# Performance work log

Measured on AMD Instinct MI355X. Metric: run time of the kernel, lower is better.

## Reference

```python
import jax, jax.numpy as jnp
import numpy as np

DIM_Q = 512
DIM_K = 512
D_Q4 = float(DIM_Q) ** 0.25  # torch: dim_q ** (1/4)
D_K4 = float(DIM_K) ** 0.25


def setup_inputs() -> dict:
    key = jax.random.key(0)
    ks = jax.random.split(key, 9)
    B, N, D_IN = 8, 4096, 512
    s_in = 1.0 / np.sqrt(D_IN)
    return {
        "x_q": jax.random.normal(ks[0], (B, N, D_IN), jnp.float32),
        "x_k": jax.random.normal(ks[1], (B, N, D_IN), jnp.float32),
        "x_v": jax.random.normal(ks[2], (B, N, D_IN), jnp.float32),
        # Linear params stored as [in, out] for x @ W + b
        "W_q": jax.random.uniform(ks[3], (D_IN, DIM_Q), jnp.float32, -s_in, s_in),
        "b_q": jax.random.uniform(ks[4], (DIM_Q,), jnp.float32, -s_in, s_in),
        "W_k": jax.random.uniform(ks[5], (D_IN, DIM_K), jnp.float32, -s_in, s_in),
        "b_k": jax.random.uniform(ks[6], (DIM_K,), jnp.float32, -s_in, s_in),
        "W_v": jax.random.uniform(ks[7], (D_IN, DIM_K), jnp.float32, -s_in, s_in),
        "b_v": jax.random.uniform(ks[8], (DIM_K,), jnp.float32, -s_in, s_in),
    }


def reference(x_q, x_k, x_v, W_q, b_q, W_k, b_k, W_v, b_v):
    Q = x_q @ W_q + b_q          # [B, n, dq]
    K = x_k @ W_k + b_k          # [B, n, dk]
    V = x_v @ W_v + b_v          # [B, n, dk]
    # softmax_row: over sequence axis (dim=-2) of Q
    A = jax.nn.softmax(Q / D_Q4, axis=-2)          # [B, n, dq]
    # softmax_col on K^T (dim=-1) == softmax over sequence axis of K
    Ks = jax.nn.softmax(K / D_K4, axis=-2)         # [B, n, dk]
    Bm = jnp.einsum("bnd,bne->bde", Ks, V)        # [B, dk, dk]
    Z = jnp.einsum("bnd,bde->bne", A, Bm)         # [B, n, dk]
    return Z
```

## Files before the change

### kernel.cpp

```cpp
#include <hip/hip_runtime.h>
#include <hip/hip_bf16.h>


typedef __bf16 bf16_t;
typedef __attribute__((ext_vector_type(8))) __bf16 bf16x8;
typedef __attribute__((ext_vector_type(4))) float f32x4;

#define MFMA_BF16 __builtin_amdgcn_mfma_f32_16x16x32_bf16

__device__ inline void async_ld16(const void* g, void* l) {
  __builtin_amdgcn_global_load_lds(
      (const __attribute__((address_space(1))) void*)g,
      (__attribute__((address_space(3))) void*)l, 16, 0, 0);
}

#define INV_D4 0.2102241038134287f

__global__ __launch_bounds__(256) void wt_kernel(
    const float* __restrict__ Wq, const float* __restrict__ Wk,
    const float* __restrict__ Wv, bf16_t* __restrict__ Wt) {
  const int z = blockIdx.z;
  const float* W = (z == 0) ? Wq : (z == 1) ? Wk : Wv;
  bf16_t* O = Wt + (size_t)z * 262144;
  __shared__ __align__(16) bf16_t tile[64 * 72];
  const int t = threadIdx.x;
  const int r = t >> 2;
  const int c4 = (t & 3) * 16;
  const int in0 = blockIdx.x * 64, out0 = blockIdx.y * 64;
  const float* src = W + (size_t)(in0 + r) * 512 + out0 + c4;
#pragma unroll
  for (int i = 0; i < 4; ++i) {
    float4 f = ((const float4*)src)[i];
    tile[(c4 + i * 4 + 0) * 72 + r] = (__bf16)f.x;
    tile[(c4 + i * 4 + 1) * 72 + r] = (__bf16)f.y;
    tile[(c4 + i * 4 + 2) * 72 + r] = (__bf16)f.z;
    tile[(c4 + i * 4 + 3) * 72 + r] = (__bf16)f.w;
  }
  __syncthreads();
  bf16x8* dst = (bf16x8*)(O + (size_t)(out0 + r) * 512 + in0 + c4);
  const bf16x8* s = (const bf16x8*)(tile + r * 72 + c4);
  dst[0] = s[0];
  dst[1] = s[1];
}

__global__ __launch_bounds__(256, 2) void proj_q(
    const float* __restrict__ Xq, const bf16_t* __restrict__ Wt,
    const float* __restrict__ bias, bf16_t* __restrict__ Eq,
    float* __restrict__ Sq) {
  __shared__ __align__(16) bf16_t Xs[4096];
  __shared__ __align__(16) bf16_t Ws[8192];

  const int t = threadIdx.x;
  const int lane = t & 63, w = t >> 6;
  const int quad = lane >> 4, l15 = lane & 15;
  const int m0 = blockIdx.x * 128;
  const int n0 = blockIdx.y * 256;
  const int m_off = (w & 1) * 64, n_off = (w >> 1) * 128;

  f32x4 acc[4][8];
  const f32x4 zero4 = {0.f, 0.f, 0.f, 0.f};
#pragma unroll
  for (int i = 0; i < 4; ++i)
#pragma unroll
    for (int j = 0; j < 8; ++j) acc[i][j] = zero4;

  const int ar = t >> 1;
  const int ac = (t & 1) * 16;
  const float* abase = Xq + (size_t)(m0 + ar) * 512 + ac;

  float4 f0 = ((const float4*)abase)[0];
  float4 f1 = ((const float4*)abase)[1];
  float4 f2 = ((const float4*)abase)[2];
  float4 f3 = ((const float4*)abase)[3];

  for (int ks = 0; ks < 16; ++ks) {
    bf16x8 p0, p1;
    p0[0] = (__bf16)f0.x; p0[1] = (__bf16)f0.y; p0[2] = (__bf16)f0.z; p0[3] = (__bf16)f0.w;
    p0[4] = (__bf16)f1.x; p0[5] = (__bf16)f1.y; p0[6] = (__bf16)f1.z; p0[7] = (__bf16)f1.w;
    p1[0] = (__bf16)f2.x; p1[1] = (__bf16)f2.y; p1[2] = (__bf16)f2.z; p1[3] = (__bf16)f2.w;
    p1[4] = (__bf16)f3.x; p1[5] = (__bf16)f3.y; p1[6] = (__bf16)f3.z; p1[7] = (__bf16)f3.w;
    ((bf16x8*)Xs)[(ac >> 3) * 128 + ar] = p0;
    ((bf16x8*)Xs)[((ac >> 3) + 1) * 128 + ar] = p1;

#pragma unroll
    for (int i = 0; i < 4; ++i) {
      const int j = w * 4 + i;
      const int k8 = j >> 2;
      const int r = ((j & 3) << 6) + lane;
      async_ld16(Wt + (size_t)(n0 + r) * 512 + ks * 32 + k8 * 8, Ws + j * 512);
    }
    __syncthreads();

    bf16x8 af[4], bfr[8];
#pragma unroll
    for (int mi = 0; mi < 4; ++mi)
      af[mi] = ((const bf16x8*)Xs)[quad * 128 + m_off + mi * 16 + l15];
#pragma unroll
    for (int ni = 0; ni < 8; ++ni)
      bfr[ni] = ((const bf16x8*)Ws)[quad * 256 + n_off + ni * 16 + l15];

    if (ks < 15) {
      const float4* p = (const float4*)(abase + (ks + 1) * 32);
      f0 = p[0]; f1 = p[1]; f2 = p[2]; f3 = p[3];
    }

#pragma unroll
    for (int mi = 0; mi < 4; ++mi)
#pragma unroll
      for (int ni = 0; ni < 8; ++ni)
        acc[mi][ni] = MFMA_BF16(af[mi], bfr[ni], acc[mi][ni], 0, 0, 0);
    __syncthreads();
  }

  const int b = m0 >> 12;
  float cs[8];
#pragma unroll
  for (int ni = 0; ni < 8; ++ni) cs[ni] = 0.f;
#pragma unroll
  for (int ni = 0; ni < 8; ++ni) {
    const int col = n0 + n_off + ni * 16 + l15;
    const float bv_ = bias[col];
#pragma unroll
    for (int mi = 0; mi < 4; ++mi)
#pragma unroll
      for (int r = 0; r < 4; ++r) {
        const int row = m0 + m_off + mi * 16 + quad * 4 + r;
        float v = __expf((acc[mi][ni][r] + bv_) * INV_D4);
        Eq[(size_t)row * 512 + col] = (bf16_t)v;
        cs[ni] += v;
      }
  }
#pragma unroll
  for (int ni = 0; ni < 8; ++ni) {
    cs[ni] += __shfl_xor(cs[ni], 16);
    cs[ni] += __shfl_xor(cs[ni], 32);
  }
  if (lane < 16) {
#pragma unroll
    for (int ni = 0; ni < 8; ++ni)
      atomicAdd(&Sq[b * 512 + n0 + n_off + ni * 16 + lane], cs[ni]);
  }
}

__global__ __launch_bounds__(256, 2) void proj_kv(
    const float* __restrict__ xk, const float* __restrict__ xv,
    const bf16_t* __restrict__ Wt, const float* __restrict__ bk,
    const float* __restrict__ bv, bf16_t* __restrict__ Ft,
    bf16_t* __restrict__ Vt) {
  const int z = blockIdx.z + 1;
  const float* X = (z == 1) ? xk : xv;
  const float* bias = (z == 1) ? bk : bv;
  const bf16_t* W = Wt + (size_t)z * 262144;
  bf16_t* Out = (z == 1) ? Ft : Vt;
  const bool expm = (z == 1);

  __shared__ __align__(16) bf16_t Xs[4096];
  __shared__ __align__(16) bf16_t Ws[8192];

  const int t = threadIdx.x;
  const int lane = t & 63, w = t >> 6;
  const int quad = lane >> 4, l15 = lane & 15;
  const int ng = blockIdx.x * 128;
  const int w0 = blockIdx.y * 256;
  const int m_off = (w & 1) * 128, n_off = (w >> 1) * 64;

  f32x4 acc[8][4];
  const f32x4 zero4 = {0.f, 0.f, 0.f, 0.f};
#pragma unroll
  for (int i = 0; i < 8; ++i)
#pragma unroll
    for (int j = 0; j < 4; ++j) acc[i][j] = zero4;

  const int br = t >> 1;
  const int bc = (t & 1) * 16;
  const float* bbase = X + (size_t)(ng + br) * 512 + bc;

  float4 f0 = ((const float4*)bbase)[0];
  float4 f1 = ((const float4*)bbase)[1];
  float4 f2 = ((const float4*)bbase)[2];
  float4 f3 = ((const float4*)bbase)[3];

  for (int ks = 0; ks < 16; ++ks) {
    bf16x8 p0, p1;
    p0[0] = (__bf16)f0.x; p0[1] = (__bf16)f0.y; p0[2] = (__bf16)f0.z; p0[3] = (__bf16)f0.w;
    p0[4] = (__bf16)f1.x; p0[5] = (__bf16)f1.y; p0[6] = (__bf16)f1.z; p0[7] = (__bf16)f1.w;
    p1[0] = (__bf16)f2.x; p1[1] = (__bf16)f2.y; p1[2] = (__bf16)f2.z; p1[3] = (__bf16)f2.w;
    p1[4] = (__bf16)f3.x; p1[5] = (__bf16)f3.y; p1[6] = (__bf16)f3.z; p1[7] = (__bf16)f3.w;
    ((bf16x8*)Xs)[(bc >> 3) * 128 + br] = p0;
    ((bf16x8*)Xs)[((bc >> 3) + 1) * 128 + br] = p1;

#pragma unroll
    for (int i = 0; i < 4; ++i) {
      const int j = w * 4 + i;
      const int k8 = j >> 2;
      const int r = ((j & 3) << 6) + lane;
      async_ld16(W + (size_t)(w0 + r) * 512 + ks * 32 + k8 * 8, Ws + j * 512);
    }
    __syncthreads();

    bf16x8 af[8], bfr[4];
#pragma unroll
    for (int mi = 0; mi < 8; ++mi)
      af[mi] = ((const bf16x8*)Ws)[quad * 256 + m_off + mi * 16 + l15];
#pragma unroll
    for (int ni = 0; ni < 4; ++ni)
      bfr[ni] = ((const bf16x8*)Xs)[quad * 128 + n_off + ni * 16 + l15];

    if (ks < 15) {
      const float4* p = (const float4*)(bbase + (ks + 1) * 32);
      f0 = p[0]; f1 = p[1]; f2 = p[2]; f3 = p[3];
    }

#pragma unroll
    for (int mi = 0; mi < 8; ++mi)
#pragma unroll
      for (int ni = 0; ni < 4; ++ni)
        acc[mi][ni] = MFMA_BF16(af[mi], bfr[ni], acc[mi][ni], 0, 0, 0);
    __syncthreads();
  }

  const int b = ng >> 12;
  const int nl0 = (ng & 4095) + n_off;
#pragma unroll
  for (int mi = 0; mi < 8; ++mi)
#pragma unroll
    for (int r = 0; r < 4; ++r) {
      const int d = w0 + m_off + mi * 16 + quad * 4 + r;
      const float bv_ = bias[d];
      bf16_t* rowp = Out + (size_t)b * 2097152 + (size_t)d * 4096 + nl0;
#pragma unroll
      for (int ni = 0; ni < 4; ++ni) {
        float v = acc[mi][ni][r] + bv_;
        if (expm) v = __expf(v * INV_D4);
        rowp[ni * 16 + l15] = (bf16_t)v;
      }
    }
}

__global__ __launch_bounds__(256) void sk_kernel(const bf16_t* __restrict__ Ft,
                                                 float* __restrict__ Sk) {
  const int row = blockIdx.x * 4 + (threadIdx.x >> 6);
  const int lane = threadIdx.x & 63;
  const bf16x8* p = (const bf16x8*)(Ft + (size_t)row * 4096) + lane;
  float s = 0.f;
#pragma unroll
  for (int j = 0; j < 8; ++j) {
    bf16x8 v = p[j * 64];
#pragma unroll
    for (int e = 0; e < 8; ++e) s += (float)v[e];
  }
#pragma unroll
  for (int m = 1; m <= 32; m <<= 1) s += __shfl_xor(s, m);
  if (lane == 0) Sk[row] = s;
}

__global__ __launch_bounds__(256, 2) void bm_gemm(
    const bf16_t* __restrict__ Ft, const bf16_t* __restrict__ Vt,
    float* __restrict__ Bmp) {
  const int b = blockIdx.z >> 1;
  const int s = blockIdx.z & 1;
  const int d0 = blockIdx.x * 128;
  const int e0 = blockIdx.y * 128;
  const bf16_t* A = Ft + (size_t)b * 2097152;
  const bf16_t* B = Vt + (size_t)b * 2097152;
  float* out = Bmp + ((size_t)s * 8 + b) * 262144;

  __shared__ __align__(16) bf16_t As[4096];
  __shared__ __align__(16) bf16_t Bs[4096];

  const int t = threadIdx.x;
  const int lane = t & 63, w = t >> 6;
  const int quad = lane >> 4, l15 = lane & 15;
  const int m_off = (w & 1) * 64, n_off = (w >> 1) * 64;

  f32x4 acc[4][4];
  const f32x4 zero4 = {0.f, 0.f, 0.f, 0.f};
#pragma unroll
  for (int i = 0; i < 4; ++i)
#pragma unroll
    for (int j = 0; j < 4; ++j) acc[i][j] = zero4;

  for (int ks = 0; ks < 64; ++ks) {
    const int k0 = s * 2048 + ks * 32;
#pragma unroll
    for (int i = 0; i < 2; ++i) {
      const int j = w * 2 + i;
      const int k8 = j >> 1;
      const int r = ((j & 1) << 6) + lane;
      async_ld16(A + (size_t)(d0 + r) * 4096 + k0 + k8 * 8, As + j * 512);
      async_ld16(B + (size_t)(e0 + r) * 4096 + k0 + k8 * 8, Bs + j * 512);
    }
    __syncthreads();
    bf16x8 af[4], bfr[4];
#pragma unroll
    for (int mi = 0; mi < 4; ++mi)
      af[mi] = ((const bf16x8*)As)[quad * 128 + m_off + mi * 16 + l15];
#pragma unroll
    for (int ni = 0; ni < 4; ++ni)
      bfr[ni] = ((const bf16x8*)Bs)[quad * 128 + n_off + ni * 16 + l15];
#pragma unroll
    for (int mi = 0; mi < 4; ++mi)
#pragma unroll
      for (int ni = 0; ni < 4; ++ni)
        acc[mi][ni] = MFMA_BF16(af[mi], bfr[ni], acc[mi][ni], 0, 0, 0);
    __syncthreads();
  }

#pragma unroll
  for (int mi = 0; mi < 4; ++mi)
#pragma unroll
    for (int ni = 0; ni < 4; ++ni) {
      const int ecol = e0 + n_off + ni * 16 + l15;
#pragma unroll
      for (int r = 0; r < 4; ++r) {
        const int drow = d0 + m_off + mi * 16 + quad * 4 + r;
        out[(size_t)drow * 512 + ecol] = acc[mi][ni][r];
      }
    }
}

__global__ __launch_bounds__(256) void scale_kernel(
    const float* __restrict__ Bmp, const float* __restrict__ Sq,
    const float* __restrict__ Sk, bf16_t* __restrict__ Ct) {
  const int b = blockIdx.z;
  const int d0 = blockIdx.x * 64, e0 = blockIdx.y * 64;
  __shared__ __align__(16) bf16_t tile[64 * 72];
  const int t = threadIdx.x;
  const int r = t >> 2;
  const int c4 = (t & 3) * 16;
  const int d = d0 + r;
  const float f = 1.0f / (Sq[b * 512 + d] * Sk[b * 512 + d]);
  const float* p0 = Bmp + (size_t)b * 262144 + (size_t)d * 512 + e0 + c4;
  const float* p1 = p0 + 2097152;
#pragma unroll
  for (int i = 0; i < 4; ++i) {
    float4 v0 = ((const float4*)p0)[i];
    float4 v1 = ((const float4*)p1)[i];
    tile[(c4 + i * 4 + 0) * 72 + r] = (__bf16)((v0.x + v1.x) * f);
    tile[(c4 + i * 4 + 1) * 72 + r] = (__bf16)((v0.y + v1.y) * f);
    tile[(c4 + i * 4 + 2) * 72 + r] = (__bf16)((v0.z + v1.z) * f);
    tile[(c4 + i * 4 + 3) * 72 + r] = (__bf16)((v0.w + v1.w) * f);
  }
  __syncthreads();
  bf16x8* dst = (bf16x8*)(Ct + (size_t)b * 262144 + (size_t)(e0 + r) * 512 + d0 + c4);
  const bf16x8* s = (const bf16x8*)(tile + r * 72 + c4);
  dst[0] = s[0];
  dst[1] = s[1];
}

__global__ __launch_bounds__(256, 2) void z_gemm(
    const bf16_t* __restrict__ Eq, const bf16_t* __restrict__ Ct,
    float* __restrict__ out) {
  __shared__ __align__(16) bf16_t As[4096];
  __shared__ __align__(16) bf16_t Bs[8192];

  const int t = threadIdx.x;
  const int lane = t & 63, w = t >> 6;
  const int quad = lane >> 4, l15 = lane & 15;
  const int m0 = blockIdx.x * 128;
  const int n0 = blockIdx.y * 256;
  const int batch = m0 >> 12;
  const bf16_t* Bt = Ct + (size_t)batch * 262144;
  const int m_off = (w & 1) * 64, n_off = (w >> 1) * 128;

  f32x4 acc[4][8];
  const f32x4 zero4 = {0.f, 0.f, 0.f, 0.f};
#pragma unroll
  for (int i = 0; i < 4; ++i)
#pragma unroll
    for (int j = 0; j < 8; ++j) acc[i][j] = zero4;

  for (int ks = 0; ks < 16; ++ks) {
    const int k0 = ks * 32;
#pragma unroll
    for (int i = 0; i < 2; ++i) {
      const int j = w * 2 + i;
      const int k8 = j >> 1;
      const int r = ((j & 1) << 6) + lane;
      async_ld16(Eq + (size_t)(m0 + r) * 512 + k0 + k8 * 8, As + j * 512);
    }
#pragma unroll
    for (int i = 0; i < 4; ++i) {
      const int j = w * 4 + i;
      const int k8 = j >> 2;
      const int r = ((j & 3) << 6) + lane;
      async_ld16(Bt + (size_t)(n0 + r) * 512 + k0 + k8 * 8, Bs + j * 512);
    }
    __syncthreads();
    bf16x8 af[4], bfr[8];
#pragma unroll
    for (int mi = 0; mi < 4; ++mi)
      af[mi] = ((const bf16x8*)As)[quad * 128 + m_off + mi * 16 + l15];
#pragma unroll
    for (int ni = 0; ni < 8; ++ni)
      bfr[ni] = ((const bf16x8*)Bs)[quad * 256 + n_off + ni * 16 + l15];
#pragma unroll
    for (int mi = 0; mi < 4; ++mi)
#pragma unroll
      for (int ni = 0; ni < 8; ++ni)
        acc[mi][ni] = MFMA_BF16(af[mi], bfr[ni], acc[mi][ni], 0, 0, 0);
    __syncthreads();
  }

#pragma unroll
  for (int mi = 0; mi < 4; ++mi)
#pragma unroll
    for (int ni = 0; ni < 8; ++ni) {
      const int col = n0 + n_off + ni * 16 + l15;
#pragma unroll
      for (int r = 0; r < 4; ++r) {
        const int row = m0 + m_off + mi * 16 + quad * 4 + r;
        out[(size_t)row * 512 + col] = acc[mi][ni][r];
      }
    }
}

extern "C" void kernel_launch(void* const* d_in, const int* in_sizes, int n_in,
                              void* d_out, int out_size, void* d_ws,
                              size_t ws_size, hipStream_t stream) {
  const float* xq = (const float*)d_in[0];
  const float* xk = (const float*)d_in[1];
  const float* xv = (const float*)d_in[2];
  const float* Wq = (const float*)d_in[3];
  const float* bq = (const float*)d_in[4];
  const float* Wk = (const float*)d_in[5];
  const float* bk = (const float*)d_in[6];
  const float* Wv = (const float*)d_in[7];
  const float* bv = (const float*)d_in[8];
  float* out = (float*)d_out;

  char* ws = (char*)d_ws;
  bf16_t* Eq = (bf16_t*)(ws + 0);
  bf16_t* Ft = (bf16_t*)(ws + 33554432);
  bf16_t* Vt = (bf16_t*)(ws + 67108864);
  float* Bmp = (float*)(ws + 100663296);
  bf16_t* Wt = (bf16_t*)(ws + 117440512);
  float* Sq = (float*)(ws + 119013376);
  float* Sk = (float*)(ws + 119029760);
  bf16_t* Ct = (bf16_t*)(ws + 33554432);

  hipMemsetAsync(Sq, 0, 16384, stream);

  wt_kernel<<<dim3(8, 8, 3), 256, 0, stream>>>(Wq, Wk, Wv, Wt);
  proj_q<<<dim3(256, 2), 256, 0, stream>>>(xq, Wt, bq, Eq, Sq);
  proj_kv<<<dim3(256, 2, 2), 256, 0, stream>>>(xk, xv, Wt, bk, bv, Ft, Vt);
  sk_kernel<<<dim3(1024), 256, 0, stream>>>(Ft, Sk);
  bm_gemm<<<dim3(4, 4, 16), 256, 0, stream>>>(Ft, Vt, Bmp);
  scale_kernel<<<dim3(8, 8, 8), 256, 0, stream>>>(Bmp, Sq, Sk, Ct);
  z_gemm<<<dim3(256, 2), 256, 0, stream>>>(Eq, Ct, out);
}
```

Measured before the change: 389.7 us.

## Double-buffer GEMM mainloops, load weights to registers, widen split-K in bm_gemm

The three projection-style GEMMs (proj_q, proj_kv, z_gemm) now read weight fragments straight from global memory into registers instead of staging them in LDS. They also double-buffer the activation tile in LDS with a two-step register prefetch, so only one barrier is needed per k-step. bm_gemm gets double-buffered async LDS loads and a split-K factor that rises to 4 when the workspace is large enough, with scale_kernel summing a variable number of partials. The aim is to hide global-load latency and raise occupancy/parallelism, at the cost of more registers and redundant weight loads across blocks.

```diff
diff --git a/kernel.cpp b/kernel.cpp
--- a/kernel.cpp
+++ b/kernel.cpp
@@ -15,6 +15,30 @@
 }
 
 #define INV_D4 0.2102241038134287f
+
+#define BAR_LGKM()                                        \
+  do {                                                    \
+    asm volatile("s_waitcnt lgkmcnt(0)" ::: "memory");    \
+    __builtin_amdgcn_s_barrier();                         \
+  } while (0)
+
+#define BAR_VM_LGKM()                                             \
+  do {                                                            \
+    asm volatile("s_waitcnt vmcnt(0) lgkmcnt(0)" ::: "memory");   \
+    __builtin_amdgcn_s_barrier();                                 \
+  } while (0)
+
+__device__ inline void cvt_store(bf16_t* dst, int c0, int ar, const float4& f0,
+                                 const float4& f1, const float4& f2,
+                                 const float4& f3) {
+  bf16x8 p0, p1;
+  p0[0] = (__bf16)f0.x; p0[1] = (__bf16)f0.y; p0[2] = (__bf16)f0.z; p0[3] = (__bf16)f0.w;
+  p0[4] = (__bf16)f1.x; p0[5] = (__bf16)f1.y; p0[6] = (__bf16)f1.z; p0[7] = (__bf16)f1.w;
+  p1[0] = (__bf16)f2.x; p1[1] = (__bf16)f2.y; p1[2] = (__bf16)f2.z; p1[3] = (__bf16)f2.w;
+  p1[4] = (__bf16)f3.x; p1[5] = (__bf16)f3.y; p1[6] = (__bf16)f3.z; p1[7] = (__bf16)f3.w;
+  ((bf16x8*)dst)[c0 * 128 + ar] = p0;
+  ((bf16x8*)dst)[(c0 + 1) * 128 + ar] = p1;
+}
 
 __global__ __launch_bounds__(256) void wt_kernel(
     const float* __restrict__ Wq, const float* __restrict__ Wk,
@@ -47,98 +71,97 @@
     const float* __restrict__ Xq, const bf16_t* __restrict__ Wt,
     const float* __restrict__ bias, bf16_t* __restrict__ Eq,
     float* __restrict__ Sq) {
-  __shared__ __align__(16) bf16_t Xs[4096];
-  __shared__ __align__(16) bf16_t Ws[8192];
+  __shared__ __align__(16) bf16_t Xs[2][4096];
 
   const int t = threadIdx.x;
   const int lane = t & 63, w = t >> 6;
   const int quad = lane >> 4, l15 = lane & 15;
   const int m0 = blockIdx.x * 128;
-  const int n0 = blockIdx.y * 256;
-  const int m_off = (w & 1) * 64, n_off = (w >> 1) * 128;
-
-  f32x4 acc[4][8];
+  const int n0 = blockIdx.y * 256 + w * 64;
+
+  f32x4 acc[8][4];
   const f32x4 zero4 = {0.f, 0.f, 0.f, 0.f};
 #pragma unroll
-  for (int i = 0; i < 4; ++i)
-#pragma unroll
-    for (int j = 0; j < 8; ++j) acc[i][j] = zero4;
+  for (int i = 0; i < 8; ++i)
+#pragma unroll
+    for (int j = 0; j < 4; ++j) acc[i][j] = zero4;
 
   const int ar = t >> 1;
-  const int ac = (t & 1) * 16;
-  const float* abase = Xq + (size_t)(m0 + ar) * 512 + ac;
-
-  float4 f0 = ((const float4*)abase)[0];
-  float4 f1 = ((const float4*)abase)[1];
-  float4 f2 = ((const float4*)abase)[2];
-  float4 f3 = ((const float4*)abase)[3];
-
+  const int c0 = (t & 1) * 2;
+  const float* abase = Xq + (size_t)(m0 + ar) * 512 + (t & 1) * 16;
+  const bf16_t* wbase = Wt + (size_t)(n0 + l15) * 512 + quad * 8;
+
+  float4 fb[2][4];
+  bf16x8 wr[2][4];
+
+  {
+    const float4* p = (const float4*)abase;
+    fb[1][0] = p[0]; fb[1][1] = p[1]; fb[1][2] = p[2]; fb[1][3] = p[3];
+  }
+#pragma unroll
+  for (int ni = 0; ni < 4; ++ni)
+    wr[0][ni] = *(const bf16x8*)(wbase + ni * 8192);
+  {
+    const float4* p = (const float4*)(abase + 32);
+    fb[0][0] = p[0]; fb[0][1] = p[1]; fb[0][2] = p[2]; fb[0][3] = p[3];
+  }
+  cvt_store(Xs[0], c0, ar, fb[1][0], fb[1][1], fb[1][2], fb[1][3]);
+  {
+    const float4* p = (const float4*)(abase + 64);
+    fb[1][0] = p[0]; fb[1][1] = p[1]; fb[1][2] = p[2]; fb[1][3] = p[3];
+  }
+  BAR_LGKM();
+
+#pragma unroll
   for (int ks = 0; ks < 16; ++ks) {
-    bf16x8 p0, p1;
-    p0[0] = (__bf16)f0.x; p0[1] = (__bf16)f0.y; p0[2] = (__bf16)f0.z; p0[3] = (__bf16)f0.w;
-    p0[4] = (__bf16)f1.x; p0[5] = (__bf16)f1.y; p0[6] = (__bf16)f1.z; p0[7] = (__bf16)f1.w;
-    p1[0] = (__bf16)f2.x; p1[1] = (__bf16)f2.y; p1[2] = (__bf16)f2.z; p1[3] = (__bf16)f2.w;
-    p1[4] = (__bf16)f3.x; p1[5] = (__bf16)f3.y; p1[6] = (__bf16)f3.z; p1[7] = (__bf16)f3.w;
-    ((bf16x8*)Xs)[(ac >> 3) * 128 + ar] = p0;
-    ((bf16x8*)Xs)[((ac >> 3) + 1) * 128 + ar] = p1;
-
-#pragma unroll
-    for (int i = 0; i < 4; ++i) {
-      const int j = w * 4 + i;
-      const int k8 = j >> 2;
-      const int r = ((j & 3) << 6) + lane;
-      async_ld16(Wt + (size_t)(n0 + r) * 512 + ks * 32 + k8 * 8, Ws + j * 512);
-    }
-    __syncthreads();
-
-    bf16x8 af[4], bfr[8];
-#pragma unroll
-    for (int mi = 0; mi < 4; ++mi)
-      af[mi] = ((const bf16x8*)Xs)[quad * 128 + m_off + mi * 16 + l15];
-#pragma unroll
-    for (int ni = 0; ni < 8; ++ni)
-      bfr[ni] = ((const bf16x8*)Ws)[quad * 256 + n_off + ni * 16 + l15];
-
+    const int p = ks & 1;
+    bf16x8 af[8];
+#pragma unroll
+    for (int mi = 0; mi < 8; ++mi)
+      af[mi] = ((const bf16x8*)Xs[p])[quad * 128 + mi * 16 + l15];
     if (ks < 15) {
-      const float4* p = (const float4*)(abase + (ks + 1) * 32);
-      f0 = p[0]; f1 = p[1]; f2 = p[2]; f3 = p[3];
-    }
-
-#pragma unroll
-    for (int mi = 0; mi < 4; ++mi)
-#pragma unroll
-      for (int ni = 0; ni < 8; ++ni)
-        acc[mi][ni] = MFMA_BF16(af[mi], bfr[ni], acc[mi][ni], 0, 0, 0);
-    __syncthreads();
+      cvt_store(Xs[p ^ 1], c0, ar, fb[p][0], fb[p][1], fb[p][2], fb[p][3]);
+#pragma unroll
+      for (int ni = 0; ni < 4; ++ni)
+        wr[p ^ 1][ni] = *(const bf16x8*)(wbase + ni * 8192 + (ks + 1) * 32);
+      if (ks < 13) {
+        const float4* pp = (const float4*)(abase + (ks + 3) * 32);
+        fb[p][0] = pp[0]; fb[p][1] = pp[1]; fb[p][2] = pp[2]; fb[p][3] = pp[3];
+      }
+    }
+#pragma unroll
+    for (int mi = 0; mi < 8; ++mi)
+#pragma unroll
+      for (int ni = 0; ni < 4; ++ni)
+        acc[mi][ni] = MFMA_BF16(af[mi], wr[p][ni], acc[mi][ni], 0, 0, 0);
+    if (ks < 15) BAR_LGKM();
   }
 
   const int b = m0 >> 12;
-  float cs[8];
-#pragma unroll
-  for (int ni = 0; ni < 8; ++ni) cs[ni] = 0.f;
-#pragma unroll
-  for (int ni = 0; ni < 8; ++ni) {
-    const int col = n0 + n_off + ni * 16 + l15;
+  float cs[4] = {0.f, 0.f, 0.f, 0.f};
+#pragma unroll
+  for (int ni = 0; ni < 4; ++ni) {
+    const int col = n0 + ni * 16 + l15;
     const float bv_ = bias[col];
 #pragma unroll
-    for (int mi = 0; mi < 4; ++mi)
+    for (int mi = 0; mi < 8; ++mi)
 #pragma unroll
       for (int r = 0; r < 4; ++r) {
-        const int row = m0 + m_off + mi * 16 + quad * 4 + r;
+        const int row = m0 + mi * 16 + quad * 4 + r;
         float v = __expf((acc[mi][ni][r] + bv_) * INV_D4);
         Eq[(size_t)row * 512 + col] = (bf16_t)v;
         cs[ni] += v;
       }
   }
 #pragma unroll
-  for (int ni = 0; ni < 8; ++ni) {
+  for (int ni = 0; ni < 4; ++ni) {
     cs[ni] += __shfl_xor(cs[ni], 16);
     cs[ni] += __shfl_xor(cs[ni], 32);
   }
   if (lane < 16) {
 #pragma unroll
-    for (int ni = 0; ni < 8; ++ni)
-      atomicAdd(&Sq[b * 512 + n0 + n_off + ni * 16 + lane], cs[ni]);
+    for (int ni = 0; ni < 4; ++ni)
+      atomicAdd(&Sq[b * 512 + n0 + ni * 16 + lane], cs[ni]);
   }
 }
 
@@ -154,82 +177,83 @@
   bf16_t* Out = (z == 1) ? Ft : Vt;
   const bool expm = (z == 1);
 
-  __shared__ __align__(16) bf16_t Xs[4096];
-  __shared__ __align__(16) bf16_t Ws[8192];
+  __shared__ __align__(16) bf16_t Xs[2][4096];
 
   const int t = threadIdx.x;
   const int lane = t & 63, w = t >> 6;
   const int quad = lane >> 4, l15 = lane & 15;
   const int ng = blockIdx.x * 128;
-  const int w0 = blockIdx.y * 256;
-  const int m_off = (w & 1) * 128, n_off = (w >> 1) * 64;
-
-  f32x4 acc[8][4];
+  const int d0 = blockIdx.y * 256 + w * 64;
+
+  f32x4 acc[4][8];
   const f32x4 zero4 = {0.f, 0.f, 0.f, 0.f};
 #pragma unroll
-  for (int i = 0; i < 8; ++i)
-#pragma unroll
-    for (int j = 0; j < 4; ++j) acc[i][j] = zero4;
-
-  const int br = t >> 1;
-  const int bc = (t & 1) * 16;
-  const float* bbase = X + (size_t)(ng + br) * 512 + bc;
-
-  float4 f0 = ((const float4*)bbase)[0];
-  float4 f1 = ((const float4*)bbase)[1];
-  float4 f2 = ((const float4*)bbase)[2];
-  float4 f3 = ((const float4*)bbase)[3];
-
+  for (int i = 0; i < 4; ++i)
+#pragma unroll
+    for (int j = 0; j < 8; ++j) acc[i][j] = zero4;
+
+  const int ar = t >> 1;
+  const int c0 = (t & 1) * 2;
+  const float* bbase = X + (size_t)(ng + ar) * 512 + (t & 1) * 16;
+  const bf16_t* wbase = W + (size_t)(d0 + l15) * 512 + quad * 8;
+
+  float4 fb[2][4];
+  bf16x8 wr[2][4];
+
+  {
+    const float4* p = (const float4*)bbase;
+    fb[1][0] = p[0]; fb[1][1] = p[1]; fb[1][2] = p[2]; fb[1][3] = p[3];
+  }
+#pragma unroll
+  for (int mi = 0; mi < 4; ++mi)
+    wr[0][mi] = *(const bf16x8*)(wbase + mi * 8192);
+  {
+    const float4* p = (const float4*)(bbase + 32);
+    fb[0][0] = p[0]; fb[0][1] = p[1]; fb[0][2] = p[2]; fb[0][3] = p[3];
+  }
+  cvt_store(Xs[0], c0, ar, fb[1][0], fb[1][1], fb[1][2], fb[1][3]);
+  {
+    const float4* p = (const float4*)(bbase + 64);
+    fb[1][0] = p[0]; fb[1][1] = p[1]; fb[1][2] = p[2]; fb[1][3] = p[3];
+  }
+  BAR_LGKM();
+
+#pragma unroll
   for (int ks = 0; ks < 16; ++ks) {
-    bf16x8 p0, p1;
-    p0[0] = (__bf16)f0.x; p0[1] = (__bf16)f0.y; p0[2] = (__bf16)f0.z; p0[3] = (__bf16)f0.w;
-    p0[4] = (__bf16)f1.x; p0[5] = (__bf16)f1.y; p0[6] = (__bf16)f1.z; p0[7] = (__bf16)f1.w;
-    p1[0] = (__bf16)f2.x; p1[1] = (__bf16)f2.y; p1[2] = (__bf16)f2.z; p1[3] = (__bf16)f2.w;
-    p1[4] = (__bf16)f3.x; p1[5] = (__bf16)f3.y; p1[6] = (__bf16)f3.z; p1[7] = (__bf16)f3.w;
-    ((bf16x8*)Xs)[(bc >> 3) * 128 + br] = p0;
-    ((bf16x8*)Xs)[((bc >> 3) + 1) * 128 + br] = p1;
-
-#pragma unroll
-    for (int i = 0; i < 4; ++i) {
-      const int j = w * 4 + i;
-      const int k8 = j >> 2;
-      const int r = ((j & 3) << 6) + lane;
-      async_ld16(W + (size_t)(w0 + r) * 512 + ks * 32 + k8 * 8, Ws + j * 512);
-    }
-    __syncthreads();
-
-    bf16x8 af[8], bfr[4];
-#pragma unroll
-    for (int mi = 0; mi < 8; ++mi)
-      af[mi] = ((const bf16x8*)Ws)[quad * 256 + m_off + mi * 16 + l15];
-#pragma unroll
-    for (int ni = 0; ni < 4; ++ni)
-      bfr[ni] = ((const bf16x8*)Xs)[quad * 128 + n_off + ni * 16 + l15];
-
+    const int p = ks & 1;
+    bf16x8 bx[8];
+#pragma unroll
+    for (int ni = 0; ni < 8; ++ni)
+      bx[ni] = ((const bf16x8*)Xs[p])[quad * 128 + ni * 16 + l15];
     if (ks < 15) {
-      const float4* p = (const float4*)(bbase + (ks + 1) * 32);
-      f0 = p[0]; f1 = p[1]; f2 = p[2]; f3 = p[3];
-    }
-
-#pragma unroll
-    for (int mi = 0; mi < 8; ++mi)
-#pragma unroll
-      for (int ni = 0; ni < 4; ++ni)
-        acc[mi][ni] = MFMA_BF16(af[mi], bfr[ni], acc[mi][ni], 0, 0, 0);
-    __syncthreads();
+      cvt_store(Xs[p ^ 1], c0, ar, fb[p][0], fb[p][1], fb[p][2], fb[p][3]);
+#pragma unroll
+      for (int mi = 0; mi < 4; ++mi)
+        wr[p ^ 1][mi] = *(const bf16x8*)(wbase + mi * 8192 + (ks + 1) * 32);
+      if (ks < 13) {
+        const float4* pp = (const float4*)(bbase + (ks + 3) * 32);
+        fb[p][0] = pp[0]; fb[p][1] = pp[1]; fb[p][2] = pp[2]; fb[p][3] = pp[3];
+      }
+    }
+#pragma unroll
+    for (int mi = 0; mi < 4; ++mi)
+#pragma unroll
+      for (int ni = 0; ni < 8; ++ni)
+        acc[mi][ni] = MFMA_BF16(wr[p][mi], bx[ni], acc[mi][ni], 0, 0, 0);
+    if (ks < 15) BAR_LGKM();
   }
 
   const int b = ng >> 12;
-  const int nl0 = (ng & 4095) + n_off;
-#pragma unroll
-  for (int mi = 0; mi < 8; ++mi)
+  const int nl0 = (ng & 4095);
+#pragma unroll
+  for (int mi = 0; mi < 4; ++mi)
 #pragma unroll
     for (int r = 0; r < 4; ++r) {
-      const int d = w0 + m_off + mi * 16 + quad * 4 + r;
+      const int d = d0 + mi * 16 + quad * 4 + r;
       const float bv_ = bias[d];
       bf16_t* rowp = Out + (size_t)b * 2097152 + (size_t)d * 4096 + nl0;
 #pragma unroll
-      for (int ni = 0; ni < 4; ++ni) {
+      for (int ni = 0; ni < 8; ++ni) {
         float v = acc[mi][ni][r] + bv_;
         if (expm) v = __expf(v * INV_D4);
         rowp[ni * 16 + l15] = (bf16_t)v;
@@ -256,23 +280,27 @@
 
 __global__ __launch_bounds__(256, 2) void bm_gemm(
     const bf16_t* __restrict__ Ft, const bf16_t* __restrict__ Vt,
-    float* __restrict__ Bmp) {
-  const int b = blockIdx.z >> 1;
-  const int s = blockIdx.z & 1;
+    float* __restrict__ Bmp, int S) {
+  const int b = blockIdx.z / S;
+  const int s = blockIdx.z - b * S;
   const int d0 = blockIdx.x * 128;
   const int e0 = blockIdx.y * 128;
   const bf16_t* A = Ft + (size_t)b * 2097152;
   const bf16_t* B = Vt + (size_t)b * 2097152;
   float* out = Bmp + ((size_t)s * 8 + b) * 262144;
 
-  __shared__ __align__(16) bf16_t As[4096];
-  __shared__ __align__(16) bf16_t Bs[4096];
+  __shared__ __align__(16) bf16_t As[2][4096];
+  __shared__ __align__(16) bf16_t Bs[2][4096];
 
   const int t = threadIdx.x;
   const int lane = t & 63, w = t >> 6;
   const int quad = lane >> 4, l15 = lane & 15;
   const int m_off = (w & 1) * 64, n_off = (w >> 1) * 64;
 
+  const int kper = 4096 / S;
+  const int KS = kper >> 5;
+  const int kbase = s * kper;
+
   f32x4 acc[4][4];
   const f32x4 zero4 = {0.f, 0.f, 0.f, 0.f};
 #pragma unroll
@@ -280,30 +308,38 @@
 #pragma unroll
     for (int j = 0; j < 4; ++j) acc[i][j] = zero4;
 
-  for (int ks = 0; ks < 64; ++ks) {
-    const int k0 = s * 2048 + ks * 32;
+  const int j0 = w * 2;
+  auto stage = [&](int buf, int ks) {
 #pragma unroll
     for (int i = 0; i < 2; ++i) {
-      const int j = w * 2 + i;
+      const int j = j0 + i;
       const int k8 = j >> 1;
       const int r = ((j & 1) << 6) + lane;
-      async_ld16(A + (size_t)(d0 + r) * 4096 + k0 + k8 * 8, As + j * 512);
-      async_ld16(B + (size_t)(e0 + r) * 4096 + k0 + k8 * 8, Bs + j * 512);
-    }
-    __syncthreads();
+      const int kel = kbase + ks * 32 + k8 * 8;
+      async_ld16(A + (size_t)(d0 + r) * 4096 + kel, &As[buf][j * 512]);
+      async_ld16(B + (size_t)(e0 + r) * 4096 + kel, &Bs[buf][j * 512]);
+    }
+  };
+
+  stage(0, 0);
+  BAR_VM_LGKM();
+
+  for (int ks = 0; ks < KS; ++ks) {
+    const int p = ks & 1;
+    if (ks + 1 < KS) stage(p ^ 1, ks + 1);
     bf16x8 af[4], bfr[4];
 #pragma unroll
     for (int mi = 0; mi < 4; ++mi)
-      af[mi] = ((const bf16x8*)As)[quad * 128 + m_off + mi * 16 + l15];
+      af[mi] = ((const bf16x8*)As[p])[quad * 128 + m_off + mi * 16 + l15];
 #pragma unroll
     for (int ni = 0; ni < 4; ++ni)
-      bfr[ni] = ((const bf16x8*)Bs)[quad * 128 + n_off + ni * 16 + l15];
+      bfr[ni] = ((const bf16x8*)Bs[p])[quad * 128 + n_off + ni * 16 + l15];
 #pragma unroll
     for (int mi = 0; mi < 4; ++mi)
 #pragma unroll
       for (int ni = 0; ni < 4; ++ni)
         acc[mi][ni] = MFMA_BF16(af[mi], bfr[ni], acc[mi][ni], 0, 0, 0);
-    __syncthreads();
+    if (ks + 1 < KS) BAR_VM_LGKM();
   }
 
 #pragma unroll
@@ -321,7 +357,7 @@
 
 __global__ __launch_bounds__(256) void scale_kernel(
     const float* __restrict__ Bmp, const float* __restrict__ Sq,
-    const float* __restrict__ Sk, bf16_t* __restrict__ Ct) {
+    const float* __restrict__ Sk, bf16_t* __restrict__ Ct, int S) {
   const int b = blockIdx.z;
   const int d0 = blockIdx.x * 64, e0 = blockIdx.y * 64;
   __shared__ __align__(16) bf16_t tile[64 * 72];
@@ -331,85 +367,100 @@
   const int d = d0 + r;
   const float f = 1.0f / (Sq[b * 512 + d] * Sk[b * 512 + d]);
   const float* p0 = Bmp + (size_t)b * 262144 + (size_t)d * 512 + e0 + c4;
-  const float* p1 = p0 + 2097152;
 #pragma unroll
   for (int i = 0; i < 4; ++i) {
-    float4 v0 = ((const float4*)p0)[i];
-    float4 v1 = ((const float4*)p1)[i];
-    tile[(c4 + i * 4 + 0) * 72 + r] = (__bf16)((v0.x + v1.x) * f);
-    tile[(c4 + i * 4 + 1) * 72 + r] = (__bf16)((v0.y + v1.y) * f);
-    tile[(c4 + i * 4 + 2) * 72 + r] = (__bf16)((v0.z + v1.z) * f);
-    tile[(c4 + i * 4 + 3) * 72 + r] = (__bf16)((v0.w + v1.w) * f);
+    float sx = 0.f, sy = 0.f, sz = 0.f, sw = 0.f;
+    for (int sp = 0; sp < S; ++sp) {
+      float4 v = ((const float4*)(p0 + (size_t)sp * 2097152))[i];
+      sx += v.x; sy += v.y; sz += v.z; sw += v.w;
+    }
+    tile[(c4 + i * 4 + 0) * 72 + r] = (__bf16)(sx * f);
+    tile[(c4 + i * 4 + 1) * 72 + r] = (__bf16)(sy * f);
+    tile[(c4 + i * 4 + 2) * 72 + r] = (__bf16)(sz * f);
+    tile[(c4 + i * 4 + 3) * 72 + r] = (__bf16)(sw * f);
   }
   __syncthreads();
   bf16x8* dst = (bf16x8*)(Ct + (size_t)b * 262144 + (size_t)(e0 + r) * 512 + d0 + c4);
-  const bf16x8* s = (const bf16x8*)(tile + r * 72 + c4);
-  dst[0] = s[0];
-  dst[1] = s[1];
+  const bf16x8* sptr = (const bf16x8*)(tile + r * 72 + c4);
+  dst[0] = sptr[0];
+  dst[1] = sptr[1];
 }
 
 __global__ __launch_bounds__(256, 2) void z_gemm(
     const bf16_t* __restrict__ Eq, const bf16_t* __restrict__ Ct,
     float* __restrict__ out) {
-  __shared__ __align__(16) bf16_t As[4096];
-  __shared__ __align__(16) bf16_t Bs[8192];
+  __shared__ __align__(16) bf16_t Xs[2][4096];
 
   const int t = threadIdx.x;
   const int lane = t & 63, w = t >> 6;
   const int quad = lane >> 4, l15 = lane & 15;
   const int m0 = blockIdx.x * 128;
-  const int n0 = blockIdx.y * 256;
+  const int n0 = blockIdx.y * 256 + w * 64;
   const int batch = m0 >> 12;
   const bf16_t* Bt = Ct + (size_t)batch * 262144;
-  const int m_off = (w & 1) * 64, n_off = (w >> 1) * 128;
-
-  f32x4 acc[4][8];
+
+  f32x4 acc[8][4];
   const f32x4 zero4 = {0.f, 0.f, 0.f, 0.f};
 #pragma unroll
-  for (int i = 0; i < 4; ++i)
-#pragma unroll
-    for (int j = 0; j < 8; ++j) acc[i][j] = zero4;
-
+  for (int i = 0; i < 8; ++i)
+#pragma unroll
+    for (int j = 0; j < 4; ++j) acc[i][j] = zero4;
+
+  const int ar = t >> 1;
+  const int c0 = (t & 1) * 2;
+  const bf16_t* abase = Eq + (size_t)(m0 + ar) * 512 + (t & 1) * 16;
+  const bf16_t* wbase = Bt + (size_t)(n0 + l15) * 512 + quad * 8;
+
+  bf16x8 eb[2][2];
+  bf16x8 wr[2][4];
+
+  eb[1][0] = *(const bf16x8*)abase;
+  eb[1][1] = *(const bf16x8*)(abase + 8);
+#pragma unroll
+  for (int ni = 0; ni < 4; ++ni)
+    wr[0][ni] = *(const bf16x8*)(wbase + ni * 8192);
+  eb[0][0] = *(const bf16x8*)(abase + 32);
+  eb[0][1] = *(const bf16x8*)(abase + 40);
+  ((bf16x8*)Xs[0])[c0 * 128 + ar] = eb[1][0];
+  ((bf16x8*)Xs[0])[(c0 + 1) * 128 + ar] = eb[1][1];
+  eb[1][0] = *(const bf16x8*)(abase + 64);
+  eb[1][1] = *(const bf16x8*)(abase + 72);
+  BAR_LGKM();
+
+#pragma unroll
   for (int ks = 0; ks < 16; ++ks) {
-    const int k0 = ks * 32;
-#pragma unroll
-    for (int i = 0; i < 2; ++i) {
-      const int j = w * 2 + i;
-      const int k8 = j >> 1;
-      const int r = ((j & 1) << 6) + lane;
-      async_ld16(Eq + (size_t)(m0 + r) * 512 + k0 + k8 * 8, As + j * 512);
-    }
-#pragma unroll
-    for (int i = 0; i < 4; ++i) {
-      const int j = w * 4 + i;
-      const int k8 = j >> 2;
-      const int r = ((j & 3) << 6) + lane;
-      async_ld16(Bt + (size_t)(n0 + r) * 512 + k0 + k8 * 8, Bs + j * 512);
-    }
-    __syncthreads();
-    bf16x8 af[4], bfr[8];
-#pragma unroll
-    for (int mi = 0; mi < 4; ++mi)
-      af[mi] = ((const bf16x8*)As)[quad * 128 + m_off + mi * 16 + l15];
-#pragma unroll
-    for (int ni = 0; ni < 8; ++ni)
-      bfr[ni] = ((const bf16x8*)Bs)[quad * 256 + n_off + ni * 16 + l15];
-#pragma unroll
-    for (int mi = 0; mi < 4; ++mi)
-#pragma unroll
-      for (int ni = 0; ni < 8; ++ni)
-        acc[mi][ni] = MFMA_BF16(af[mi], bfr[ni], acc[mi][ni], 0, 0, 0);
-    __syncthreads();
-  }
-
-#pragma unroll
-  for (int mi = 0; mi < 4; ++mi)
-#pragma unroll
-    for (int ni = 0; ni < 8; ++ni) {
-      const int col = n0 + n_off + ni * 16 + l15;
+    const int p = ks & 1;
+    bf16x8 af[8];
+#pragma unroll
+    for (int mi = 0; mi < 8; ++mi)
+      af[mi] = ((const bf16x8*)Xs[p])[quad * 128 + mi * 16 + l15];
+    if (ks < 15) {
+      ((bf16x8*)Xs[p ^ 1])[c0 * 128 + ar] = eb[p][0];
+      ((bf16x8*)Xs[p ^ 1])[(c0 + 1) * 128 + ar] = eb[p][1];
+#pragma unroll
+      for (int ni = 0; ni < 4; ++ni)
+        wr[p ^ 1][ni] = *(const bf16x8*)(wbase + ni * 8192 + (ks + 1) * 32);
+      if (ks < 13) {
+        eb[p][0] = *(const bf16x8*)(abase + (ks + 3) * 32);
+        eb[p][1] = *(const bf16x8*)(abase + (ks + 3) * 32 + 8);
+      }
+    }
+#pragma unroll
+    for (int mi = 0; mi < 8; ++mi)
+#pragma unroll
+      for (int ni = 0; ni < 4; ++ni)
+        acc[mi][ni] = MFMA_BF16(af[mi], wr[p][ni], acc[mi][ni], 0, 0, 0);
+    if (ks < 15) BAR_LGKM();
+  }
+
+#pragma unroll
+  for (int mi = 0; mi < 8; ++mi)
+#pragma unroll
+    for (int ni = 0; ni < 4; ++ni) {
+      const int col = n0 + ni * 16 + l15;
 #pragma unroll
       for (int r = 0; r < 4; ++r) {
-        const int row = m0 + m_off + mi * 16 + quad * 4 + r;
+        const int row = m0 + mi * 16 + quad * 4 + r;
         out[(size_t)row * 512 + col] = acc[mi][ni][r];
       }
     }
@@ -434,9 +485,12 @@
   bf16_t* Ft = (bf16_t*)(ws + 33554432);
   bf16_t* Vt = (bf16_t*)(ws + 67108864);
   float* Bmp = (float*)(ws + 100663296);
-  bf16_t* Wt = (bf16_t*)(ws + 117440512);
-  float* Sq = (float*)(ws + 119013376);
-  float* Sk = (float*)(ws + 119029760);
+
+  const int S = (ws_size >= (size_t)135823360) ? 4 : 2;
+  const size_t wt_off = (S == 4) ? (size_t)134217728 : (size_t)117440512;
+  bf16_t* Wt = (bf16_t*)(ws + wt_off);
+  float* Sq = (float*)(ws + wt_off + 1572864);
+  float* Sk = (float*)(ws + wt_off + 1572864 + 16384);
   bf16_t* Ct = (bf16_t*)(ws + 33554432);
 
   hipMemsetAsync(Sq, 0, 16384, stream);
@@ -445,7 +499,7 @@
   proj_q<<<dim3(256, 2), 256, 0, stream>>>(xq, Wt, bq, Eq, Sq);
   proj_kv<<<dim3(256, 2, 2), 256, 0, stream>>>(xk, xv, Wt, bk, bv, Ft, Vt);
   sk_kernel<<<dim3(1024), 256, 0, stream>>>(Ft, Sk);
-  bm_gemm<<<dim3(4, 4, 16), 256, 0, stream>>>(Ft, Vt, Bmp);
-  scale_kernel<<<dim3(8, 8, 8), 256, 0, stream>>>(Bmp, Sq, Sk, Ct);
+  bm_gemm<<<dim3(4, 4, 8 * S), 256, 0, stream>>>(Ft, Vt, Bmp, S);
+  scale_kernel<<<dim3(8, 8, 8), 256, 0, stream>>>(Bmp, Sq, Sk, Ct, S);
   z_gemm<<<dim3(256, 2), 256, 0, stream>>>(Eq, Ct, out);
 }
```

Result: faster. 378.0 us (-3.0%).
